# Kernel tuning notes

Hardware: AMD Instinct MI355X
Metric: run time of the kernel (lower is better)

Reference implementation:

```python
import jax, jax.numpy as jnp
import numpy as np

MARGIN = 0.3


def setup_inputs() -> dict:
    key = jax.random.key(0)
    k1, k2 = jax.random.split(key)
    N, D = 8192, 128
    embeddings = jax.random.normal(k1, (N, D), dtype=jnp.float32)
    labels = jax.random.randint(k2, (N,), 0, 512, dtype=jnp.int64)
    return {"embeddings": embeddings, "labels": labels}


def _pairwise_dist(x):
    # Euclidean cdist via squared-norm expansion; safe sqrt (zero grad at d==0).
    sq_norms = jnp.sum(x * x, axis=-1)  # [N]
    sq = sq_norms[:, None] + sq_norms[None, :] - 2.0 * (x @ x.T)  # [N, N]
    sq = jnp.maximum(sq, 0.0)
    safe = jnp.where(sq > 0.0, sq, 1.0)
    return jnp.where(sq > 0.0, jnp.sqrt(safe), 0.0)


def reference(embeddings, labels):
    d = _pairwise_dist(embeddings)  # [N, N]
    same = labels[:, None] == labels[None, :]
    eye = jnp.eye(labels.shape[0], dtype=bool)
    pos_mask = same & ~eye
    neg_mask = ~same

    inf = jnp.float32(jnp.inf)
    hardest_pos = jnp.max(jnp.where(pos_mask, d, -inf), axis=1)  # [N]
    hardest_neg = jnp.min(jnp.where(neg_mask, d, inf), axis=1)   # [N]

    valid = jnp.any(pos_mask, axis=1) & jnp.any(neg_mask, axis=1)
    per_row = jax.nn.relu(hardest_pos - hardest_neg + MARGIN)
    per_row = jnp.where(valid, per_row, 0.0)
    count = jnp.sum(valid)
    return jnp.where(count > 0, jnp.sum(per_row) / jnp.maximum(count, 1), 0.0)
```

## Files before the change

kernel.cpp:

```cpp
#include <hip/hip_runtime.h>
#include <hip/hip_fp16.h>

#define N 8192
#define D 128
#define MARGIN 0.3f

typedef __fp16 half_t;
typedef __attribute__((ext_vector_type(8))) __fp16 half8;
typedef __attribute__((ext_vector_type(4))) float f32x4;

#define AS1C(p) ((const __attribute__((address_space(1))) void*)(p))
#define AS3(p)  ((__attribute__((address_space(3))) void*)(p))

__global__ void triplet_prep(const float* __restrict__ x,
                             half_t* __restrict__ xh,
                             float* __restrict__ norms,
                             float* __restrict__ gacc) {
    const int gt = blockIdx.x * 256 + threadIdx.x;
    if (gt < 3) gacc[gt] = 0.f;
    const int row  = gt >> 6;
    const int lane = gt & 63;
    const float* rp = x + (size_t)row * D;
    float a0 = rp[lane], a1 = rp[lane + 64];
    xh[(size_t)row * D + lane]      = (half_t)a0;
    xh[(size_t)row * D + lane + 64] = (half_t)a1;
    float s = fmaf(a0, a0, a1 * a1);
#pragma unroll
    for (int o = 32; o > 0; o >>= 1) s += __shfl_xor(s, o);
    if (lane == 0) norms[row] = s;
}

__launch_bounds__(256, 2)
__global__ void triplet_main(const half_t* __restrict__ xh,
                             const float* __restrict__ norms,
                             const int* __restrict__ labels,
                             float* __restrict__ ppos,
                             float* __restrict__ pneg) {
    __shared__ __align__(16) half_t S[2][128 * D];

    const int bx    = blockIdx.x;
    const int strip = bx >> 3;
    const int chunk = bx & 7;
    const int tid   = threadIdx.x;
    const int lane  = tid & 63;
    const int w     = tid >> 6;
    const int wr    = w >> 1;
    const int wc    = w & 1;
    const int lrow  = lane >> 4;
    const int lcol  = lane & 15;
    const int irow0 = strip * 128;

    const int ssl   = (tid & 15) ^ ((tid >> 4) & 7);
    const int sgoff = (tid >> 4) * D + ssl * 8;
    const int sldst = tid * 8;

    const int ibase = irow0 + wr * 64 + lrow * 4;
    int li[16];
#pragma unroll
    for (int fi = 0; fi < 4; ++fi)
#pragma unroll
        for (int rg = 0; rg < 4; ++rg)
            li[fi * 4 + rg] = labels[ibase + fi * 16 + rg];

#pragma unroll
    for (int it = 0; it < 8; ++it)
        __builtin_amdgcn_global_load_lds(AS1C(xh + (size_t)(irow0 + it * 16) * D + sgoff),
                                         AS3(&S[0][it * 2048 + sldst]), 16, 0, 0);
    const int jchunk0 = chunk * 1024;
#pragma unroll
    for (int it = 0; it < 8; ++it)
        __builtin_amdgcn_global_load_lds(AS1C(xh + (size_t)(jchunk0 + it * 16) * D + sgoff),
                                         AS3(&S[1][it * 2048 + sldst]), 16, 0, 0);
    asm volatile("s_waitcnt vmcnt(0)" ::: "memory");
    __builtin_amdgcn_s_barrier();
    __builtin_amdgcn_sched_barrier(0);

    int physk[4];
#pragma unroll
    for (int ks = 0; ks < 4; ++ks) physk[ks] = ((ks * 4 + lrow) ^ (lcol & 7)) * 8;
    half8 af[4][4];
#pragma unroll
    for (int fi = 0; fi < 4; ++fi) {
        const half_t* ap = &S[0][(wr * 64 + fi * 16 + lcol) * D];
#pragma unroll
        for (int ks = 0; ks < 4; ++ks)
            af[fi][ks] = *(const half8*)(ap + physk[ks]);
    }
    asm volatile("s_waitcnt lgkmcnt(0)" ::: "memory");
    __builtin_amdgcn_sched_barrier(0);
    __builtin_amdgcn_s_barrier();
    __builtin_amdgcn_sched_barrier(0);

    int rowB[4];
#pragma unroll
    for (int f4 = 0; f4 < 4; ++f4) rowB[f4] = (wc * 64 + f4 * 16 + lcol) * D;

    float mpos[16], mneg[16];
#pragma unroll
    for (int r = 0; r < 16; ++r) { mpos[r] = -1e38f; mneg[r] = 1e38f; }

    const half_t* Bcur  = &S[1][0];
    half_t*       Bnext = &S[0][0];

    for (int jt = 0; jt < 8; ++jt) {
        const int jbase = jchunk0 + jt * 128;

        if (jt < 7) {
            const int nb = jbase + 128;
#pragma unroll
            for (int it = 0; it < 8; ++it)
                __builtin_amdgcn_global_load_lds(AS1C(xh + (size_t)(nb + it * 16) * D + sgoff),
                                                 AS3(Bnext + it * 2048 + sldst), 16, 0, 0);
        }

        int lj[4]; float njv[4];
#pragma unroll
        for (int fj = 0; fj < 4; ++fj) {
            int j = jbase + wc * 64 + fj * 16 + lcol;
            lj[fj]  = labels[j];
            njv[fj] = norms[j];
        }

        f32x4 acc[4][4];
#pragma unroll
        for (int fi = 0; fi < 4; ++fi)
#pragma unroll
            for (int fj = 0; fj < 4; ++fj)
                acc[fi][fj] = (f32x4){0.f, 0.f, 0.f, 0.f};

#pragma unroll
        for (int ks = 0; ks < 4; ++ks) {
            half8 bv[4];
#pragma unroll
            for (int fj = 0; fj < 4; ++fj)
                bv[fj] = *(const half8*)(Bcur + rowB[fj] + physk[ks]);
#pragma unroll
            for (int fi = 0; fi < 4; ++fi)
#pragma unroll
                for (int fj = 0; fj < 4; ++fj)
                    acc[fi][fj] = __builtin_amdgcn_mfma_f32_16x16x32_f16(
                        af[fi][ks], bv[fj], acc[fi][fj], 0, 0, 0);
        }

        const bool hasdiag = (jbase == irow0);
        const int jcolbase = jbase + wc * 64 + lcol;
#pragma unroll
        for (int fi = 0; fi < 4; ++fi) {
#pragma unroll
            for (int fj = 0; fj < 4; ++fj) {
#pragma unroll
                for (int rg = 0; rg < 4; ++rg) {
                    float cand = fmaf(-2.f, acc[fi][fj][rg], njv[fj]);
                    int r = fi * 4 + rg;
                    bool same = (li[r] == lj[fj]);
                    bool pos = same;
                    if (hasdiag) {
                        int ig = ibase + fi * 16 + rg;
                        int jg = jcolbase + fj * 16;
                        pos = same && (ig != jg);
                    }
                    if (pos)   mpos[r] = fmaxf(mpos[r], cand);
                    if (!same) mneg[r] = fminf(mneg[r], cand);
                }
            }
        }

        asm volatile("s_waitcnt vmcnt(0)" ::: "memory");
        __builtin_amdgcn_s_barrier();
        __builtin_amdgcn_sched_barrier(0);
        const half_t* t = Bcur; Bcur = Bnext; Bnext = (half_t*)t;
    }

#pragma unroll
    for (int o = 1; o < 16; o <<= 1) {
#pragma unroll
        for (int r = 0; r < 16; ++r) {
            mpos[r] = fmaxf(mpos[r], __shfl_xor(mpos[r], o));
            mneg[r] = fminf(mneg[r], __shfl_xor(mneg[r], o));
        }
    }
    if (lcol == 0) {
        const int slot = chunk * 2 + wc;
#pragma unroll
        for (int fi = 0; fi < 4; ++fi)
#pragma unroll
            for (int rg = 0; rg < 4; ++rg) {
                int rgrow = ibase + fi * 16 + rg;
                ppos[(size_t)rgrow * 16 + slot] = mpos[fi * 4 + rg];
                pneg[(size_t)rgrow * 16 + slot] = mneg[fi * 4 + rg];
            }
    }
}

__global__ void triplet_reduce(const float* __restrict__ ppos,
                               const float* __restrict__ pneg,
                               const float* __restrict__ norms,
                               float* __restrict__ gacc,
                               float* __restrict__ out) {
    __shared__ float ss[256];
    __shared__ float sc[256];
    const int tid = threadIdx.x;
    const int r   = blockIdx.x * 256 + tid;
    float mp = -1e38f, mn = 1e38f;
    const f32x4* pp = (const f32x4*)(ppos + (size_t)r * 16);
    const f32x4* pn = (const f32x4*)(pneg + (size_t)r * 16);
#pragma unroll
    for (int s4 = 0; s4 < 4; ++s4) {
        f32x4 a = pp[s4], b = pn[s4];
#pragma unroll
        for (int e = 0; e < 4; ++e) { mp = fmaxf(mp, a[e]); mn = fminf(mn, b[e]); }
    }
    float ni = norms[r];
    bool valid = (mp > -1e37f) && (mn < 1e37f);
    float hp = sqrtf(fmaxf(ni + mp, 0.f));
    float hn = sqrtf(fmaxf(ni + mn, 0.f));
    float pr = fmaxf(hp - hn + MARGIN, 0.f);
    ss[tid] = valid ? pr : 0.f;
    sc[tid] = valid ? 1.f : 0.f;
    __syncthreads();
    for (int o = 128; o > 0; o >>= 1) {
        if (tid < o) { ss[tid] += ss[tid + o]; sc[tid] += sc[tid + o]; }
        __syncthreads();
    }
    if (tid == 0) {
        atomicAdd(&gacc[0], ss[0]);
        atomicAdd(&gacc[1], sc[0]);
        __threadfence();
        unsigned* ticket = (unsigned*)(gacc + 2);
        unsigned old = atomicAdd(ticket, 1u);
        if (old == gridDim.x - 1) {
            float s = atomicAdd(&gacc[0], 0.f);
            float c = atomicAdd(&gacc[1], 0.f);
            out[0] = (c > 0.f) ? (s / c) : 0.f;
        }
    }
}

extern "C" void kernel_launch(void* const* d_in, const int* in_sizes, int n_in,
                              void* d_out, int out_size, void* d_ws, size_t ws_size,
                              hipStream_t stream) {
    const float* x      = (const float*)d_in[0];
    const int*   labels = (const int*)d_in[1];
    float*       out    = (float*)d_out;

    char*   ws    = (char*)d_ws;
    half_t* xh    = (half_t*)ws;
    float*  norms = (float*)(ws + (size_t)N * D * sizeof(half_t));
    float*  ppos  = norms + N;
    float*  pneg  = ppos + (size_t)N * 16;
    float*  gacc  = pneg + (size_t)N * 16;

    triplet_prep  <<<N / 4,   256, 0, stream>>>(x, xh, norms, gacc);
    triplet_main  <<<512,     256, 0, stream>>>(xh, norms, labels, ppos, pneg);
    triplet_reduce<<<N / 256, 256, 0, stream>>>(ppos, pneg, norms, gacc, out);
}
```

Before: 48.16 us.

## Stage labels/norms in LDS, unroll tile loop by two, mask diagonal via accumulator

Labels and norms for the whole j-chunk are loaded into shared memory once at kernel start, replacing per-tile global loads inside the loop. The tile loop is manually unrolled by two with static double-buffer pointers, and MFMA sections are wrapped in s_setprio to favor matrix issue. Diagonal exclusion is done by overwriting the diagonal accumulator entries with a large value, which makes the per-element predicate branch-free. This adds 8KB of LDS per block, which may affect occupancy at 2 blocks per CU.

```diff
diff --git a/kernel.cpp b/kernel.cpp
--- a/kernel.cpp
+++ b/kernel.cpp
@@ -30,13 +30,99 @@
     if (lane == 0) norms[row] = s;
 }
 
+struct TState {
+    float mpos[16];
+    float mneg[16];
+};
+
+__device__ __forceinline__ void tile_body(
+    const half_t* __restrict__ Scur, half_t* __restrict__ Snxt,
+    bool dopf, int pfjt, int jt,
+    const half_t* __restrict__ xh,
+    int jchunk0, int irow0, int sgoff, int sldst,
+    int wr, int wc, int lrow, int lcol,
+    const int* __restrict__ Ljs, const float* __restrict__ Njs,
+    const half8 (&af)[4][4], const int (&li)[16], const int (&rowB)[4],
+    const int (&physk)[4], TState& st)
+{
+    if (dopf) {
+        const int nb = jchunk0 + pfjt * 128;
+#pragma unroll
+        for (int it = 0; it < 8; ++it)
+            __builtin_amdgcn_global_load_lds(AS1C(xh + (size_t)(nb + it * 16) * D + sgoff),
+                                             AS3(Snxt + it * 2048 + sldst), 16, 0, 0);
+    }
+
+    const int jbase = jchunk0 + jt * 128;
+    int lj[4]; float njv[4];
+#pragma unroll
+    for (int fj = 0; fj < 4; ++fj) {
+        int idx = jt * 128 + wc * 64 + fj * 16 + lcol;
+        lj[fj]  = Ljs[idx];
+        njv[fj] = Njs[idx];
+    }
+
+    f32x4 acc[4][4];
+#pragma unroll
+    for (int fi = 0; fi < 4; ++fi)
+#pragma unroll
+        for (int fj = 0; fj < 4; ++fj)
+            acc[fi][fj] = (f32x4){0.f, 0.f, 0.f, 0.f};
+
+    __builtin_amdgcn_s_setprio(1);
+#pragma unroll
+    for (int ks = 0; ks < 4; ++ks) {
+        half8 bv[4];
+#pragma unroll
+        for (int fj = 0; fj < 4; ++fj)
+            bv[fj] = *(const half8*)(Scur + rowB[fj] + physk[ks]);
+#pragma unroll
+        for (int fi = 0; fi < 4; ++fi)
+#pragma unroll
+            for (int fj = 0; fj < 4; ++fj)
+                acc[fi][fj] = __builtin_amdgcn_mfma_f32_16x16x32_f16(
+                    af[fi][ks], bv[fj], acc[fi][fj], 0, 0, 0);
+    }
+    __builtin_amdgcn_s_setprio(0);
+
+    if (jbase == irow0) {
+        bool dl = (wr == wc) && (lrow == (lcol >> 2));
+        int  dr = lcol & 3;
+#pragma unroll
+        for (int f = 0; f < 4; ++f)
+#pragma unroll
+            for (int rg = 0; rg < 4; ++rg)
+                acc[f][f][rg] = (dl && (rg == dr)) ? 1e30f : acc[f][f][rg];
+    }
+
+#pragma unroll
+    for (int fi = 0; fi < 4; ++fi)
+#pragma unroll
+        for (int fj = 0; fj < 4; ++fj)
+#pragma unroll
+            for (int rg = 0; rg < 4; ++rg) {
+                float cand = fmaf(-2.f, acc[fi][fj][rg], njv[fj]);
+                int r = fi * 4 + rg;
+                bool same = (li[r] == lj[fj]);
+                st.mpos[r] = same ? fmaxf(st.mpos[r], cand) : st.mpos[r];
+                st.mneg[r] = same ? st.mneg[r] : fminf(st.mneg[r], cand);
+            }
+
+    asm volatile("s_waitcnt vmcnt(0)" ::: "memory");
+    __builtin_amdgcn_s_barrier();
+    __builtin_amdgcn_sched_barrier(0);
+}
+
 __launch_bounds__(256, 2)
 __global__ void triplet_main(const half_t* __restrict__ xh,
                              const float* __restrict__ norms,
                              const int* __restrict__ labels,
                              float* __restrict__ ppos,
                              float* __restrict__ pneg) {
-    __shared__ __align__(16) half_t S[2][128 * D];
+    __shared__ __align__(16) half_t S0[128 * D];
+    __shared__ __align__(16) half_t S1[128 * D];
+    __shared__ __align__(16) int    Ljs[1024];
+    __shared__ __align__(16) float  Njs[1024];
 
     const int bx    = blockIdx.x;
     const int strip = bx >> 3;
@@ -49,6 +135,7 @@
     const int lrow  = lane >> 4;
     const int lcol  = lane & 15;
     const int irow0 = strip * 128;
+    const int jchunk0 = chunk * 1024;
 
     const int ssl   = (tid & 15) ^ ((tid >> 4) & 7);
     const int sgoff = (tid >> 4) * D + ssl * 8;
@@ -65,12 +152,13 @@
 #pragma unroll
     for (int it = 0; it < 8; ++it)
         __builtin_amdgcn_global_load_lds(AS1C(xh + (size_t)(irow0 + it * 16) * D + sgoff),
-                                         AS3(&S[0][it * 2048 + sldst]), 16, 0, 0);
-    const int jchunk0 = chunk * 1024;
+                                         AS3(&S0[it * 2048 + sldst]), 16, 0, 0);
+    __builtin_amdgcn_global_load_lds(AS1C(labels + jchunk0 + tid * 4), AS3(&Ljs[tid * 4]), 16, 0, 0);
+    __builtin_amdgcn_global_load_lds(AS1C(norms  + jchunk0 + tid * 4), AS3(&Njs[tid * 4]), 16, 0, 0);
 #pragma unroll
     for (int it = 0; it < 8; ++it)
         __builtin_amdgcn_global_load_lds(AS1C(xh + (size_t)(jchunk0 + it * 16) * D + sgoff),
-                                         AS3(&S[1][it * 2048 + sldst]), 16, 0, 0);
+                                         AS3(&S1[it * 2048 + sldst]), 16, 0, 0);
     asm volatile("s_waitcnt vmcnt(0)" ::: "memory");
     __builtin_amdgcn_s_barrier();
     __builtin_amdgcn_sched_barrier(0);
@@ -81,7 +169,7 @@
     half8 af[4][4];
 #pragma unroll
     for (int fi = 0; fi < 4; ++fi) {
-        const half_t* ap = &S[0][(wr * 64 + fi * 16 + lcol) * D];
+        const half_t* ap = &S0[(wr * 64 + fi * 16 + lcol) * D];
 #pragma unroll
         for (int ks = 0; ks < 4; ++ks)
             af[fi][ks] = *(const half8*)(ap + physk[ks]);
@@ -95,88 +183,23 @@
 #pragma unroll
     for (int f4 = 0; f4 < 4; ++f4) rowB[f4] = (wc * 64 + f4 * 16 + lcol) * D;
 
-    float mpos[16], mneg[16];
-#pragma unroll
-    for (int r = 0; r < 16; ++r) { mpos[r] = -1e38f; mneg[r] = 1e38f; }
-
-    const half_t* Bcur  = &S[1][0];
-    half_t*       Bnext = &S[0][0];
-
-    for (int jt = 0; jt < 8; ++jt) {
-        const int jbase = jchunk0 + jt * 128;
-
-        if (jt < 7) {
-            const int nb = jbase + 128;
-#pragma unroll
-            for (int it = 0; it < 8; ++it)
-                __builtin_amdgcn_global_load_lds(AS1C(xh + (size_t)(nb + it * 16) * D + sgoff),
-                                                 AS3(Bnext + it * 2048 + sldst), 16, 0, 0);
-        }
-
-        int lj[4]; float njv[4];
-#pragma unroll
-        for (int fj = 0; fj < 4; ++fj) {
-            int j = jbase + wc * 64 + fj * 16 + lcol;
-            lj[fj]  = labels[j];
-            njv[fj] = norms[j];
-        }
-
-        f32x4 acc[4][4];
-#pragma unroll
-        for (int fi = 0; fi < 4; ++fi)
-#pragma unroll
-            for (int fj = 0; fj < 4; ++fj)
-                acc[fi][fj] = (f32x4){0.f, 0.f, 0.f, 0.f};
-
-#pragma unroll
-        for (int ks = 0; ks < 4; ++ks) {
-            half8 bv[4];
-#pragma unroll
-            for (int fj = 0; fj < 4; ++fj)
-                bv[fj] = *(const half8*)(Bcur + rowB[fj] + physk[ks]);
-#pragma unroll
-            for (int fi = 0; fi < 4; ++fi)
-#pragma unroll
-                for (int fj = 0; fj < 4; ++fj)
-                    acc[fi][fj] = __builtin_amdgcn_mfma_f32_16x16x32_f16(
-                        af[fi][ks], bv[fj], acc[fi][fj], 0, 0, 0);
-        }
-
-        const bool hasdiag = (jbase == irow0);
-        const int jcolbase = jbase + wc * 64 + lcol;
-#pragma unroll
-        for (int fi = 0; fi < 4; ++fi) {
-#pragma unroll
-            for (int fj = 0; fj < 4; ++fj) {
-#pragma unroll
-                for (int rg = 0; rg < 4; ++rg) {
-                    float cand = fmaf(-2.f, acc[fi][fj][rg], njv[fj]);
-                    int r = fi * 4 + rg;
-                    bool same = (li[r] == lj[fj]);
-                    bool pos = same;
-                    if (hasdiag) {
-                        int ig = ibase + fi * 16 + rg;
-                        int jg = jcolbase + fj * 16;
-                        pos = same && (ig != jg);
-                    }
-                    if (pos)   mpos[r] = fmaxf(mpos[r], cand);
-                    if (!same) mneg[r] = fminf(mneg[r], cand);
-                }
-            }
-        }
-
-        asm volatile("s_waitcnt vmcnt(0)" ::: "memory");
-        __builtin_amdgcn_s_barrier();
-        __builtin_amdgcn_sched_barrier(0);
-        const half_t* t = Bcur; Bcur = Bnext; Bnext = (half_t*)t;
+    TState st;
+#pragma unroll
+    for (int r = 0; r < 16; ++r) { st.mpos[r] = -1e38f; st.mneg[r] = 1e38f; }
+
+    for (int k = 0; k < 4; ++k) {
+        tile_body(S1, S0, true,    2 * k + 1, 2 * k,     xh, jchunk0, irow0, sgoff, sldst,
+                  wr, wc, lrow, lcol, Ljs, Njs, af, li, rowB, physk, st);
+        tile_body(S0, S1, (k < 3), 2 * k + 2, 2 * k + 1, xh, jchunk0, irow0, sgoff, sldst,
+                  wr, wc, lrow, lcol, Ljs, Njs, af, li, rowB, physk, st);
     }
 
 #pragma unroll
     for (int o = 1; o < 16; o <<= 1) {
 #pragma unroll
         for (int r = 0; r < 16; ++r) {
-            mpos[r] = fmaxf(mpos[r], __shfl_xor(mpos[r], o));
-            mneg[r] = fminf(mneg[r], __shfl_xor(mneg[r], o));
+            st.mpos[r] = fmaxf(st.mpos[r], __shfl_xor(st.mpos[r], o));
+            st.mneg[r] = fminf(st.mneg[r], __shfl_xor(st.mneg[r], o));
         }
     }
     if (lcol == 0) {
@@ -186,8 +209,8 @@
 #pragma unroll
             for (int rg = 0; rg < 4; ++rg) {
                 int rgrow = ibase + fi * 16 + rg;
-                ppos[(size_t)rgrow * 16 + slot] = mpos[fi * 4 + rg];
-                pneg[(size_t)rgrow * 16 + slot] = mneg[fi * 4 + rg];
+                ppos[(size_t)rgrow * 16 + slot] = st.mpos[fi * 4 + rg];
+                pneg[(size_t)rgrow * 16 + slot] = st.mneg[fi * 4 + rg];
             }
     }
 }
```

After: 68.26 us. 41.7% more time.

## Drop LDS staging; stream B fragments per wave from global with register prefetch

Applied to the files above, without the earlier changes.

The main kernel is restructured so that each wave independently handles 64 rows against a 512-column chunk. B fragments, labels and norms are loaded straight from global memory into registers through a three-deep rotating prefetch, which removes the shared-memory double buffer and all block barriers. The self-pair is now excluded by overwriting the diagonal dot product with a huge value instead of a per-element index compare, and MFMA sections are wrapped in setprio. In exchange, each B tile is reused by fewer rows, which roughly doubles global/L2 read traffic, and the partial-result layout changes to 16 chunks per row.

```diff
diff --git a/kernel.cpp b/kernel.cpp
--- a/kernel.cpp
+++ b/kernel.cpp
@@ -8,9 +8,6 @@
 typedef __fp16 half_t;
 typedef __attribute__((ext_vector_type(8))) __fp16 half8;
 typedef __attribute__((ext_vector_type(4))) float f32x4;
-
-#define AS1C(p) ((const __attribute__((address_space(1))) void*)(p))
-#define AS3(p)  ((__attribute__((address_space(3))) void*)(p))
 
 __global__ void triplet_prep(const float* __restrict__ x,
                              half_t* __restrict__ xh,
@@ -30,31 +27,84 @@
     if (lane == 0) norms[row] = s;
 }
 
+
+#define PF(BN, LJN, NJN, SN) {                                          \
+    const int jn = colbase + (SN) * 16 + lcol;                          \
+    const half_t* bp = xh + (size_t)jn * D + lrow * 8;                  \
+    BN[0] = *(const half8*)bp;                                          \
+    BN[1] = *(const half8*)(bp + 32);                                   \
+    BN[2] = *(const half8*)(bp + 64);                                   \
+    BN[3] = *(const half8*)(bp + 96);                                   \
+    LJN = labels[jn];                                                   \
+    NJN = norms[jn];                                                    \
+}
+
+#define POISON(ACC) {                                                   \
+    _Pragma("unroll")                                                   \
+    for (int rg = 0; rg < 4; ++rg)                                      \
+        ACC[rg] = (diagl && rg == drg) ? 1e30f : ACC[rg];               \
+}
+
+#define EPI(ACC, FI, LJC, NJC) {                                        \
+    _Pragma("unroll")                                                   \
+    for (int rg = 0; rg < 4; ++rg) {                                    \
+        float c = fmaf(-2.f, ACC[rg], (NJC));                           \
+        bool same = (li[(FI) * 4 + rg] == (LJC));                       \
+        mpos[(FI)*4+rg] = same ? fmaxf(mpos[(FI)*4+rg], c) : mpos[(FI)*4+rg]; \
+        mneg[(FI)*4+rg] = same ? mneg[(FI)*4+rg] : fminf(mneg[(FI)*4+rg], c); \
+    }                                                                   \
+}
+
+#define COMP(BC, LJC, NJC, S) {                                         \
+    f32x4 a0 = {0,0,0,0}, a1 = {0,0,0,0}, a2 = {0,0,0,0}, a3 = {0,0,0,0}; \
+    __builtin_amdgcn_s_setprio(1);                                      \
+    _Pragma("unroll")                                                   \
+    for (int ks = 0; ks < 4; ++ks) {                                    \
+        a0 = __builtin_amdgcn_mfma_f32_16x16x32_f16(af[0][ks], BC[ks], a0, 0, 0, 0); \
+        a1 = __builtin_amdgcn_mfma_f32_16x16x32_f16(af[1][ks], BC[ks], a1, 0, 0, 0); \
+        a2 = __builtin_amdgcn_mfma_f32_16x16x32_f16(af[2][ks], BC[ks], a2, 0, 0, 0); \
+        a3 = __builtin_amdgcn_mfma_f32_16x16x32_f16(af[3][ks], BC[ks], a3, 0, 0, 0); \
+    }                                                                   \
+    __builtin_amdgcn_s_setprio(0);                                      \
+    const int dj = colbase + (S) * 16 - rowbase;                        \
+    if (dj == 0)       POISON(a0)                                       \
+    else if (dj == 16) POISON(a1)                                       \
+    else if (dj == 32) POISON(a2)                                       \
+    else if (dj == 48) POISON(a3)                                       \
+    EPI(a0, 0, LJC, NJC)                                                \
+    EPI(a1, 1, LJC, NJC)                                                \
+    EPI(a2, 2, LJC, NJC)                                                \
+    EPI(a3, 3, LJC, NJC)                                                \
+}
+
 __launch_bounds__(256, 2)
 __global__ void triplet_main(const half_t* __restrict__ xh,
                              const float* __restrict__ norms,
                              const int* __restrict__ labels,
                              float* __restrict__ ppos,
                              float* __restrict__ pneg) {
-    __shared__ __align__(16) half_t S[2][128 * D];
-
-    const int bx    = blockIdx.x;
-    const int strip = bx >> 3;
-    const int chunk = bx & 7;
     const int tid   = threadIdx.x;
     const int lane  = tid & 63;
-    const int w     = tid >> 6;
-    const int wr    = w >> 1;
-    const int wc    = w & 1;
+    const int gw    = blockIdx.x * 4 + (tid >> 6);
+    const int rowg  = gw >> 4;
+    const int chunk = gw & 15;
     const int lrow  = lane >> 4;
     const int lcol  = lane & 15;
-    const int irow0 = strip * 128;
-
-    const int ssl   = (tid & 15) ^ ((tid >> 4) & 7);
-    const int sgoff = (tid >> 4) * D + ssl * 8;
-    const int sldst = tid * 8;
-
-    const int ibase = irow0 + wr * 64 + lrow * 4;
+    const int rowbase = rowg * 64;
+    const int colbase = chunk * 512;
+    const bool diagl = (lrow == (lcol >> 2));
+    const int  drg   = lcol & 3;
+
+    half8 af[4][4];
+#pragma unroll
+    for (int fi = 0; fi < 4; ++fi) {
+        const half_t* ap = xh + (size_t)(rowbase + fi * 16 + lcol) * D + lrow * 8;
+#pragma unroll
+        for (int ks = 0; ks < 4; ++ks)
+            af[fi][ks] = *(const half8*)(ap + ks * 32);
+    }
+
+    const int ibase = rowbase + lrow * 4;
     int li[16];
 #pragma unroll
     for (int fi = 0; fi < 4; ++fi)
@@ -62,114 +112,24 @@
         for (int rg = 0; rg < 4; ++rg)
             li[fi * 4 + rg] = labels[ibase + fi * 16 + rg];
 
-#pragma unroll
-    for (int it = 0; it < 8; ++it)
-        __builtin_amdgcn_global_load_lds(AS1C(xh + (size_t)(irow0 + it * 16) * D + sgoff),
-                                         AS3(&S[0][it * 2048 + sldst]), 16, 0, 0);
-    const int jchunk0 = chunk * 1024;
-#pragma unroll
-    for (int it = 0; it < 8; ++it)
-        __builtin_amdgcn_global_load_lds(AS1C(xh + (size_t)(jchunk0 + it * 16) * D + sgoff),
-                                         AS3(&S[1][it * 2048 + sldst]), 16, 0, 0);
-    asm volatile("s_waitcnt vmcnt(0)" ::: "memory");
-    __builtin_amdgcn_s_barrier();
-    __builtin_amdgcn_sched_barrier(0);
-
-    int physk[4];
-#pragma unroll
-    for (int ks = 0; ks < 4; ++ks) physk[ks] = ((ks * 4 + lrow) ^ (lcol & 7)) * 8;
-    half8 af[4][4];
-#pragma unroll
-    for (int fi = 0; fi < 4; ++fi) {
-        const half_t* ap = &S[0][(wr * 64 + fi * 16 + lcol) * D];
-#pragma unroll
-        for (int ks = 0; ks < 4; ++ks)
-            af[fi][ks] = *(const half8*)(ap + physk[ks]);
-    }
-    asm volatile("s_waitcnt lgkmcnt(0)" ::: "memory");
-    __builtin_amdgcn_sched_barrier(0);
-    __builtin_amdgcn_s_barrier();
-    __builtin_amdgcn_sched_barrier(0);
-
-    int rowB[4];
-#pragma unroll
-    for (int f4 = 0; f4 < 4; ++f4) rowB[f4] = (wc * 64 + f4 * 16 + lcol) * D;
-
     float mpos[16], mneg[16];
 #pragma unroll
     for (int r = 0; r < 16; ++r) { mpos[r] = -1e38f; mneg[r] = 1e38f; }
 
-    const half_t* Bcur  = &S[1][0];
-    half_t*       Bnext = &S[0][0];
-
-    for (int jt = 0; jt < 8; ++jt) {
-        const int jbase = jchunk0 + jt * 128;
-
-        if (jt < 7) {
-            const int nb = jbase + 128;
-#pragma unroll
-            for (int it = 0; it < 8; ++it)
-                __builtin_amdgcn_global_load_lds(AS1C(xh + (size_t)(nb + it * 16) * D + sgoff),
-                                                 AS3(Bnext + it * 2048 + sldst), 16, 0, 0);
-        }
-
-        int lj[4]; float njv[4];
-#pragma unroll
-        for (int fj = 0; fj < 4; ++fj) {
-            int j = jbase + wc * 64 + fj * 16 + lcol;
-            lj[fj]  = labels[j];
-            njv[fj] = norms[j];
-        }
-
-        f32x4 acc[4][4];
-#pragma unroll
-        for (int fi = 0; fi < 4; ++fi)
-#pragma unroll
-            for (int fj = 0; fj < 4; ++fj)
-                acc[fi][fj] = (f32x4){0.f, 0.f, 0.f, 0.f};
-
-#pragma unroll
-        for (int ks = 0; ks < 4; ++ks) {
-            half8 bv[4];
-#pragma unroll
-            for (int fj = 0; fj < 4; ++fj)
-                bv[fj] = *(const half8*)(Bcur + rowB[fj] + physk[ks]);
-#pragma unroll
-            for (int fi = 0; fi < 4; ++fi)
-#pragma unroll
-                for (int fj = 0; fj < 4; ++fj)
-                    acc[fi][fj] = __builtin_amdgcn_mfma_f32_16x16x32_f16(
-                        af[fi][ks], bv[fj], acc[fi][fj], 0, 0, 0);
-        }
-
-        const bool hasdiag = (jbase == irow0);
-        const int jcolbase = jbase + wc * 64 + lcol;
-#pragma unroll
-        for (int fi = 0; fi < 4; ++fi) {
-#pragma unroll
-            for (int fj = 0; fj < 4; ++fj) {
-#pragma unroll
-                for (int rg = 0; rg < 4; ++rg) {
-                    float cand = fmaf(-2.f, acc[fi][fj][rg], njv[fj]);
-                    int r = fi * 4 + rg;
-                    bool same = (li[r] == lj[fj]);
-                    bool pos = same;
-                    if (hasdiag) {
-                        int ig = ibase + fi * 16 + rg;
-                        int jg = jcolbase + fj * 16;
-                        pos = same && (ig != jg);
-                    }
-                    if (pos)   mpos[r] = fmaxf(mpos[r], cand);
-                    if (!same) mneg[r] = fminf(mneg[r], cand);
-                }
-            }
-        }
-
-        asm volatile("s_waitcnt vmcnt(0)" ::: "memory");
-        __builtin_amdgcn_s_barrier();
-        __builtin_amdgcn_sched_barrier(0);
-        const half_t* t = Bcur; Bcur = Bnext; Bnext = (half_t*)t;
-    }
+    half8 b0[4], b1[4], b2[4];
+    int lj0, lj1, lj2; float nj0, nj1, nj2;
+    PF(b0, lj0, nj0, 0)
+    PF(b1, lj1, nj1, 1)
+    for (int s = 0; s < 30; s += 3) {
+        PF(b2, lj2, nj2, s + 2)
+        COMP(b0, lj0, nj0, s)
+        PF(b0, lj0, nj0, s + 3)
+        COMP(b1, lj1, nj1, s + 1)
+        PF(b1, lj1, nj1, s + 4)
+        COMP(b2, lj2, nj2, s + 2)
+    }
+    COMP(b0, lj0, nj0, 30)
+    COMP(b1, lj1, nj1, 31)
 
 #pragma unroll
     for (int o = 1; o < 16; o <<= 1) {
@@ -180,14 +140,13 @@
         }
     }
     if (lcol == 0) {
-        const int slot = chunk * 2 + wc;
 #pragma unroll
         for (int fi = 0; fi < 4; ++fi)
 #pragma unroll
             for (int rg = 0; rg < 4; ++rg) {
-                int rgrow = ibase + fi * 16 + rg;
-                ppos[(size_t)rgrow * 16 + slot] = mpos[fi * 4 + rg];
-                pneg[(size_t)rgrow * 16 + slot] = mneg[fi * 4 + rg];
+                int row = ibase + fi * 16 + rg;
+                ppos[(size_t)row * 16 + chunk] = mpos[fi * 4 + rg];
+                pneg[(size_t)row * 16 + chunk] = mneg[fi * 4 + rg];
             }
     }
 }
```

Result: slower. 55.07 us (+14.3%).
